# Kernel tuning notes

Measured on AMD Instinct MI355X. Metric: run time of the kernel, lower is better.

## Reference

```python
import jax, jax.numpy as jnp
import numpy as np

D = 64
H = 4
HD = D // H
N_MOL, E_MOL = 2048, 32768
N_PROT, E_PROT = 8192, 262144
LN_EPS = 1e-5


def _lin_params(key, d_in, d_out):
    k1, k2 = jax.random.split(key)
    lim = 1.0 / np.sqrt(d_in)
    w = jax.random.uniform(k1, (d_in, d_out), minval=-lim, maxval=lim, dtype=jnp.float32)
    b = jax.random.uniform(k2, (d_out,), minval=-lim, maxval=lim, dtype=jnp.float32)
    return w, b


def setup_inputs() -> dict:
    key = jax.random.key(0)
    ks = jax.random.split(key, 20)
    inp = {
        'x_mol': jax.random.normal(ks[0], (N_MOL, D), dtype=jnp.float32),
        'edge_index_mol': jax.random.randint(ks[1], (2, E_MOL), 0, N_MOL),
        'edge_attr_mol': jax.random.normal(ks[2], (E_MOL, D), dtype=jnp.float32),
        'x_prot': jax.random.normal(ks[3], (N_PROT, D), dtype=jnp.float32),
        'edge_index_prot': jax.random.randint(ks[4], (2, E_PROT), 0, N_PROT),
        'edge_attr_prot': jax.random.normal(ks[5], (E_PROT, D), dtype=jnp.float32),
    }
    # GINE MLPs: Linear -> ReLU -> Linear
    inp['mol_w1'], inp['mol_b1'] = _lin_params(ks[6], D, D)
    inp['mol_w2'], inp['mol_b2'] = _lin_params(ks[7], D, D)
    inp['prot_w1'], inp['prot_b1'] = _lin_params(ks[8], D, D)
    inp['prot_w2'], inp['prot_b2'] = _lin_params(ks[9], D, D)
    # cross-attn mol->prot (query=mol, key/value=prot)
    inp['mp_wq'], inp['mp_bq'] = _lin_params(ks[10], D, D)
    inp['mp_wk'], inp['mp_bk'] = _lin_params(ks[11], D, D)
    inp['mp_wv'], inp['mp_bv'] = _lin_params(ks[12], D, D)
    # cross-attn prot->mol (query=prot, key/value=mol)
    inp['pm_wq'], inp['pm_bq'] = _lin_params(ks[13], D, D)
    inp['pm_wk'], inp['pm_bk'] = _lin_params(ks[14], D, D)
    inp['pm_wv'], inp['pm_bv'] = _lin_params(ks[15], D, D)
    # layer norms
    inp['ln_mol_g'] = jnp.ones((D,), jnp.float32)
    inp['ln_mol_b'] = jnp.zeros((D,), jnp.float32)
    inp['ln_prot_g'] = jnp.ones((D,), jnp.float32)
    inp['ln_prot_b'] = jnp.zeros((D,), jnp.float32)
    return inp


def _gine_conv(x, edge_index, edge_attr, w1, b1, w2, b2, n_nodes):
    # message: relu(x_j + edge_attr); aggregate: mean at target; update: MLP((1+eps)*x + aggr), eps=0
    src, dst = edge_index[0], edge_index[1]
    msg = jax.nn.relu(x[src] + edge_attr)                       # [E, D]
    ssum = jax.ops.segment_sum(msg, dst, num_segments=n_nodes)  # [N, D]
    cnt = jax.ops.segment_sum(jnp.ones((msg.shape[0],), msg.dtype), dst, num_segments=n_nodes)
    aggr = ssum / jnp.maximum(cnt, 1.0)[:, None]
    h = x + aggr
    h = jax.nn.relu(h @ w1 + b1) @ w2 + b2
    return h


def _cross_attn(q_nodes, k_nodes, wq, bq, wk, bk, wv, bv):
    Nq, Nk = q_nodes.shape[0], k_nodes.shape[0]
    Q = (q_nodes @ wq + bq).reshape(Nq, H, HD)
    K = (k_nodes @ wk + bk).reshape(Nk, H, HD)
    V = (k_nodes @ wv + bv).reshape(Nk, H, HD)
    scores = jnp.einsum('qhd,khd->hqk', Q, K) / np.sqrt(HD).astype(np.float32)
    attn = jax.nn.softmax(scores, axis=-1)                      # [H, Nq, Nk]
    out = jnp.einsum('hqk,khd->qhd', attn, V).reshape(Nq, D)
    return out


def _layer_norm(x, g, b):
    mu = jnp.mean(x, axis=-1, keepdims=True)
    var = jnp.mean(jnp.square(x - mu), axis=-1, keepdims=True)
    return (x - mu) * jax.lax.rsqrt(var + LN_EPS) * g + b


def reference(x_mol, edge_index_mol, edge_attr_mol, x_prot, edge_index_prot, edge_attr_prot,
              mol_w1, mol_b1, mol_w2, mol_b2, prot_w1, prot_b1, prot_w2, prot_b2,
              mp_wq, mp_bq, mp_wk, mp_bk, mp_wv, mp_bv,
              pm_wq, pm_bq, pm_wk, pm_bk, pm_wv, pm_bv,
              ln_mol_g, ln_mol_b, ln_prot_g, ln_prot_b):
    h_mol = jax.nn.relu(_gine_conv(x_mol, edge_index_mol, edge_attr_mol,
                                   mol_w1, mol_b1, mol_w2, mol_b2, x_mol.shape[0]))
    h_prot = jax.nn.relu(_gine_conv(x_prot, edge_index_prot, edge_attr_prot,
                                    prot_w1, prot_b1, prot_w2, prot_b2, x_prot.shape[0]))
    h_mol_attn = _cross_attn(h_mol, h_prot, mp_wq, mp_bq, mp_wk, mp_bk, mp_wv, mp_bv)
    h_prot_attn = _cross_attn(h_prot, h_mol, pm_wq, pm_bq, pm_wk, pm_bk, pm_wv, pm_bv)
    out_mol = _layer_norm(h_mol + h_mol_attn, ln_mol_g, ln_mol_b)
    out_prot = _layer_norm(h_prot + h_prot_attn, ln_prot_g, ln_prot_b)
    return out_mol, out_prot
```

## Files before the change

### kernel.cpp

```cpp
#include <hip/hip_runtime.h>

#define NM 2048
#define EM 32768
#define NP 8192
#define EP 262144

typedef __attribute__((ext_vector_type(8))) short short8;
typedef __attribute__((ext_vector_type(4))) float f32x4;

#define LOG2E 1.44269504088896340736f

__device__ __forceinline__ float e2(float x) { return __builtin_amdgcn_exp2f(x); }
__device__ __forceinline__ unsigned int pk_bf16(float a, float b) {
    unsigned int ua = __float_as_uint(a) + 0x8000u;
    unsigned int ub = __float_as_uint(b) + 0x8000u;
    return __builtin_amdgcn_perm(ua, ub, 0x03020706u);
}
__device__ __forceinline__ unsigned short cvt_bf16(float f) {
    unsigned int u = __float_as_uint(f);
    u = (u + 0x7fff + ((u >> 16) & 1)) >> 16;
    return (unsigned short)u;
}

__global__ __launch_bounds__(256) void hist_kernel(
    const int* __restrict__ ei_m, const int* __restrict__ ei_p,
    int* __restrict__ cnt_m, int* __restrict__ cnt_p)
{
    int idx = blockIdx.x * 256 + threadIdx.x;
    if (idx < EM) atomicAdd(&cnt_m[ei_m[EM + idx]], 1);
    int j = idx - EM;
    if (j >= 0 && j < EP) atomicAdd(&cnt_p[ei_p[EP + j]], 1);
}

__global__ __launch_bounds__(256) void scan_kernel(
    const int* __restrict__ cnt_m, const int* __restrict__ cnt_p,
    int* __restrict__ start_m, int* __restrict__ start_p,
    int* __restrict__ cur_m, int* __restrict__ cur_p)
{
    const int* cnt; int* start; int* cur; int n;
    if (blockIdx.x == 0) { cnt = cnt_m; start = start_m; cur = cur_m; n = NM; }
    else                 { cnt = cnt_p; start = start_p; cur = cur_p; n = NP; }
    int per = n >> 8;
    int tid = threadIdx.x;
    int base = tid * per;
    int s = 0;
    for (int i = 0; i < per; i++) s += cnt[base + i];
    __shared__ int wsum[4];
    int lane = tid & 63, w = tid >> 6;
    int v = s;
    #pragma unroll
    for (int off = 1; off < 64; off <<= 1) {
        int u = __shfl_up(v, off, 64);
        if (lane >= off) v += u;
    }
    if (lane == 63) wsum[w] = v;
    __syncthreads();
    int wo = 0;
    for (int i = 0; i < w; i++) wo += wsum[i];
    int run = wo + v - s;
    for (int i = 0; i < per; i++) {
        start[base + i] = run; cur[base + i] = run;
        run += cnt[base + i];
    }
    if (tid == 255) start[n] = run;
}

__global__ __launch_bounds__(256) void scatter_kernel(
    const int* __restrict__ ei_m, const int* __restrict__ ei_p,
    int* __restrict__ cur_m, int* __restrict__ cur_p,
    int* __restrict__ pidx_m, int* __restrict__ pidx_p)
{
    int idx = blockIdx.x * 256 + threadIdx.x;
    if (idx < EM) {
        int d = ei_m[EM + idx];
        int pos = atomicAdd(&cur_m[d], 1);
        pidx_m[pos] = (idx << 11) | ei_m[idx];
    }
    int j = idx - EM;
    if (j >= 0 && j < EP) {
        int d = ei_p[EP + j];
        int pos = atomicAdd(&cur_p[d], 1);
        pidx_p[pos] = (j << 13) | ei_p[j];
    }
}

__global__ __launch_bounds__(256) void node_aggr_kernel(
    const float* __restrict__ x_m, const float* __restrict__ ea_m,
    const int* __restrict__ start_m, const int* __restrict__ pidx_m,
    const float* __restrict__ x_p, const float* __restrict__ ea_p,
    const int* __restrict__ start_p, const int* __restrict__ pidx_p,
    float* __restrict__ h0_m, float* __restrict__ h0_p)
{
    int wave = threadIdx.x >> 6, lane = threadIdx.x & 63;
    int nid = blockIdx.x * 4 + wave;
    const float *x, *ea; const int *start, *pidx; float* h0; int n, sh, msk;
    if (nid < NM) { x = x_m; ea = ea_m; start = start_m; pidx = pidx_m; h0 = h0_m; n = nid; sh = 11; msk = 2047; }
    else          { x = x_p; ea = ea_p; start = start_p; pidx = pidx_p; h0 = h0_p; n = nid - NM; sh = 13; msk = 8191; }
    int b = start[n], e = start[n + 1];
    int deg = e - b;
    float acc = 0.f;
    for (int c0 = 0; c0 < deg; c0 += 64) {
        int rem = deg - c0;
        int mcount = rem < 64 ? rem : 64;
        int pk = 0;
        if (lane < mcount) pk = pidx[b + c0 + lane];
        int j = 0;
        for (; j + 3 < mcount; j += 4) {
            int v0 = __shfl(pk, j, 64),     v1 = __shfl(pk, j + 1, 64);
            int v2 = __shfl(pk, j + 2, 64), v3 = __shfl(pk, j + 3, 64);
            float a0 = ea[(size_t)(((unsigned)v0) >> sh) * 64 + lane];
            float a1 = ea[(size_t)(((unsigned)v1) >> sh) * 64 + lane];
            float a2 = ea[(size_t)(((unsigned)v2) >> sh) * 64 + lane];
            float a3 = ea[(size_t)(((unsigned)v3) >> sh) * 64 + lane];
            float y0 = x[(size_t)(v0 & msk) * 64 + lane];
            float y1 = x[(size_t)(v1 & msk) * 64 + lane];
            float y2 = x[(size_t)(v2 & msk) * 64 + lane];
            float y3 = x[(size_t)(v3 & msk) * 64 + lane];
            acc += fmaxf(y0 + a0, 0.f);
            acc += fmaxf(y1 + a1, 0.f);
            acc += fmaxf(y2 + a2, 0.f);
            acc += fmaxf(y3 + a3, 0.f);
        }
        for (; j < mcount; ++j) {
            int v0 = __shfl(pk, j, 64);
            acc += fmaxf(x[(size_t)(v0 & msk) * 64 + lane] + ea[(size_t)(((unsigned)v0) >> sh) * 64 + lane], 0.f);
        }
    }
    float aggr = acc / fmaxf((float)deg, 1.f);
    h0[(size_t)n * 64 + lane] = x[(size_t)n * 64 + lane] + aggr;
}

__global__ __launch_bounds__(256) void gine_mlp_kernel(
    const float* __restrict__ h0_m, const float* __restrict__ h0_p,
    const float* __restrict__ w1m, const float* __restrict__ b1m,
    const float* __restrict__ w2m, const float* __restrict__ b2m,
    const float* __restrict__ w1p, const float* __restrict__ b1p,
    const float* __restrict__ w2p, const float* __restrict__ b2p,
    float* __restrict__ hm, float* __restrict__ hp)
{
    const float *h0, *w1, *b1, *w2, *b2; float* out; int row0;
    if (blockIdx.x < NM / 16) {
        h0 = h0_m; w1 = w1m; b1 = b1m; w2 = w2m; b2 = b2m; out = hm;
        row0 = blockIdx.x * 16;
    } else {
        h0 = h0_p; w1 = w1p; b1 = b1p; w2 = w2p; b2 = b2p; out = hp;
        row0 = (blockIdx.x - NM / 16) * 16;
    }
    __shared__ float sW1[4096], sW2[4096], sb1[64], sb2[64];
    __shared__ float sh0[16][64], sh1[16][64];
    int t = threadIdx.x;
    for (int i = t; i < 4096; i += 256) { sW1[i] = w1[i]; sW2[i] = w2[i]; }
    if (t < 64) { sb1[t] = b1[t]; sb2[t] = b2[t]; }
    for (int i = t; i < 16 * 64; i += 256) {
        int r = i >> 6, c = i & 63;
        sh0[r][c] = h0[(size_t)(row0 + r) * 64 + c];
    }
    __syncthreads();
    int j = t & 63, rs = t >> 6;
    for (int r = rs; r < 16; r += 4) {
        float a = sb1[j];
        #pragma unroll
        for (int c = 0; c < 64; c++) a += sh0[r][c] * sW1[c * 64 + j];
        sh1[r][j] = fmaxf(a, 0.0f);
    }
    __syncthreads();
    for (int r = rs; r < 16; r += 4) {
        float a = sb2[j];
        #pragma unroll
        for (int c = 0; c < 64; c++) a += sh1[r][c] * sW2[c * 64 + j];
        out[(size_t)(row0 + r) * 64 + j] = fmaxf(a, 0.0f);
    }
}

__global__ __launch_bounds__(256) void qkv_bf16_kernel(
    const float* __restrict__ hm, const float* __restrict__ hp,
    const float* __restrict__ wq_m, const float* __restrict__ bq_m,
    const float* __restrict__ wk_m, const float* __restrict__ bk_m,
    const float* __restrict__ wv_m, const float* __restrict__ bv_m,
    const float* __restrict__ wq_p, const float* __restrict__ bq_p,
    const float* __restrict__ wk_p, const float* __restrict__ bk_p,
    const float* __restrict__ wv_p, const float* __restrict__ bv_p,
    unsigned short* __restrict__ Qm, unsigned short* __restrict__ Km, unsigned short* __restrict__ Vtm,
    unsigned short* __restrict__ Qp, unsigned short* __restrict__ Kp, unsigned short* __restrict__ Vtp)
{
    const float *x, *wq, *bq, *wk, *bk, *wv, *bv;
    unsigned short *Q, *K, *Vt; int row0, N;
    if (blockIdx.x < NM / 16) {
        x = hm; wq = wq_m; bq = bq_m; wk = wk_m; bk = bk_m; wv = wv_m; bv = bv_m;
        Q = Qm; K = Km; Vt = Vtm; N = NM; row0 = blockIdx.x * 16;
    } else {
        x = hp; wq = wq_p; bq = bq_p; wk = wk_p; bk = bk_p; wv = wv_p; bv = bv_p;
        Q = Qp; K = Kp; Vt = Vtp; N = NP; row0 = (blockIdx.x - NM / 16) * 16;
    }
    __shared__ float sWq[4096], sWk[4096], sWv[4096];
    __shared__ float sbq[64], sbk[64], sbv[64];
    __shared__ float sh0[16][64];
    int t = threadIdx.x;
    for (int i = t; i < 4096; i += 256) { sWq[i] = wq[i]; sWk[i] = wk[i]; sWv[i] = wv[i]; }
    if (t < 64) { sbq[t] = bq[t]; sbk[t] = bk[t]; sbv[t] = bv[t]; }
    for (int i = t; i < 16 * 64; i += 256) {
        int r = i >> 6, c = i & 63;
        sh0[r][c] = x[(size_t)(row0 + r) * 64 + c];
    }
    __syncthreads();
    int j = t & 63, rs = t >> 6;
    for (int r = rs; r < 16; r += 4) {
        float aq = sbq[j], ak = sbk[j], av = sbv[j];
        #pragma unroll
        for (int c = 0; c < 64; c++) {
            float h = sh0[r][c];
            aq += h * sWq[c * 64 + j];
            ak += h * sWk[c * 64 + j];
            av += h * sWv[c * 64 + j];
        }
        size_t o = (size_t)(row0 + r) * 64 + j;
        Q[o] = cvt_bf16(aq * (0.25f * LOG2E));
        K[o] = cvt_bf16(ak);
        Vt[(size_t)j * N + row0 + r] = cvt_bf16(av);
    }
}

__global__ __launch_bounds__(256) void attn_kernel(
    const unsigned short* __restrict__ Qm, const unsigned short* __restrict__ Km,
    const unsigned short* __restrict__ Vtm,
    const unsigned short* __restrict__ Qp, const unsigned short* __restrict__ Kp,
    const unsigned short* __restrict__ Vtp,
    float* __restrict__ partial)
{
    __shared__ unsigned int plds[4][16][20];
    int t = threadIdx.x;
    int wave = t >> 6;
    int lane = t & 63;
    int qrow = lane & 15;
    int quad = lane >> 4;
    int T = blockIdx.x * 4 + wave;

    const unsigned short *Q, *K, *Vt; int Nk, ncb, tloc;
    if (T < 4096) { Q = Qm; K = Kp; Vt = Vtp; Nk = NP; ncb = 3; tloc = T; }
    else          { Q = Qp; K = Km; Vt = Vtm; Nk = NM; ncb = 1; tloc = T - 4096; }
    int chunk = tloc & ((1 << ncb) - 1);
    int tmp = tloc >> ncb;
    int h = tmp & 3;
    int qt = tmp >> 2;

    short8 qf = {};
    if (quad < 2)
        qf = *(const short8*)(Q + ((size_t)(qt * 16 + qrow)) * 64 + h * 16 + quad * 8);

    float m = -3.0e38f, l = 0.0f;
    f32x4 acc = {0.f, 0.f, 0.f, 0.f};
    const f32x4 zero4 = {0.f, 0.f, 0.f, 0.f};
    int kbase = chunk * 1024;
    const unsigned short* vrow = Vt + ((size_t)(h * 16 + qrow)) * Nk;

    short8 kf0n = {}, kf1n = {}, vfn;
    {
        if (quad < 2) {
            kf0n = *(const short8*)(K + ((size_t)(kbase + qrow)) * 64 + h * 16 + quad * 8);
            kf1n = *(const short8*)(K + ((size_t)(kbase + 16 + qrow)) * 64 + h * 16 + quad * 8);
        }
        vfn = *(const short8*)(vrow + kbase + quad * 8);
    }

    for (int it = 0; it < 32; ++it) {
        short8 kf0 = kf0n, kf1 = kf1n, vf = vfn;
        if (it < 31) {
            int key0 = kbase + (it + 1) * 32;
            if (quad < 2) {
                kf0n = *(const short8*)(K + ((size_t)(key0 + qrow)) * 64 + h * 16 + quad * 8);
                kf1n = *(const short8*)(K + ((size_t)(key0 + 16 + qrow)) * 64 + h * 16 + quad * 8);
            }
            vfn = *(const short8*)(vrow + key0 + quad * 8);
        }

        f32x4 s0 = __builtin_amdgcn_mfma_f32_16x16x32_bf16(kf0, qf, zero4, 0, 0, 0);
        f32x4 s1 = __builtin_amdgcn_mfma_f32_16x16x32_bf16(kf1, qf, zero4, 0, 0, 0);

        float tmax = fmaxf(fmaxf(fmaxf(s0.x, s0.y), fmaxf(s0.z, s0.w)),
                           fmaxf(fmaxf(s1.x, s1.y), fmaxf(s1.z, s1.w)));
        tmax = fmaxf(tmax, __shfl_xor(tmax, 16, 64));
        tmax = fmaxf(tmax, __shfl_xor(tmax, 32, 64));
        float mnew = fmaxf(m, tmax);
        float alpha = e2(m - mnew);
        float p00 = e2(s0.x - mnew), p01 = e2(s0.y - mnew);
        float p02 = e2(s0.z - mnew), p03 = e2(s0.w - mnew);
        float p10 = e2(s1.x - mnew), p11 = e2(s1.y - mnew);
        float p12 = e2(s1.z - mnew), p13 = e2(s1.w - mnew);
        l = l * alpha + (((p00 + p01) + (p02 + p03)) + ((p10 + p11) + (p12 + p13)));
        acc.x *= alpha; acc.y *= alpha; acc.z *= alpha; acc.w *= alpha;

        uint2 w0; w0.x = pk_bf16(p00, p01); w0.y = pk_bf16(p02, p03);
        uint2 w1; w1.x = pk_bf16(p10, p11); w1.y = pk_bf16(p12, p13);
        *(uint2*)&plds[wave][qrow][quad * 2] = w0;
        *(uint2*)&plds[wave][qrow][8 + quad * 2] = w1;
        short8 pf = *(short8*)&plds[wave][qrow][quad * 4];

        acc = __builtin_amdgcn_mfma_f32_16x16x32_bf16(vf, pf, acc, 0, 0, 0);
        m = mnew;
    }

    float ltot = l + __shfl_xor(l, 16, 64);
    ltot += __shfl_xor(ltot, 32, 64);

    float* pb = partial + (size_t)T * 288;
    *(f32x4*)&pb[qrow * 16 + quad * 4] = acc;
    if (quad == 0) { pb[256 + qrow] = m; pb[272 + qrow] = ltot; }
}

__global__ __launch_bounds__(256) void merge_ln_kernel(
    const float* __restrict__ partial,
    const float* __restrict__ h_m, const float* __restrict__ h_p,
    const float* __restrict__ gm, const float* __restrict__ bm,
    const float* __restrict__ gp, const float* __restrict__ bp_,
    float* __restrict__ out)
{
    int t = threadIdx.x;
    int grow = blockIdx.x * 4 + (t >> 6);
    int c = t & 63;
    const float *pbase, *hbuf, *g, *bb; float* o; int NC, row;
    if (grow < NM) { pbase = partial;               hbuf = h_m; g = gm; bb = bm;  o = out;             NC = 8; row = grow; }
    else           { pbase = partial + 4096 * 288;  hbuf = h_p; g = gp; bb = bp_; o = out + NM * 64;   NC = 2; row = grow - NM; }
    int hi = c >> 4, d = c & 15;
    int qt = row >> 4, ql = row & 15;
    const float* base = pbase + (size_t)(qt * 4 + hi) * NC * 288;
    float M = -3.0e38f;
    for (int cc = 0; cc < NC; ++cc) M = fmaxf(M, base[cc * 288 + 256 + ql]);
    float L = 0.0f, A = 0.0f;
    for (int cc = 0; cc < NC; ++cc) {
        float w = e2(base[cc * 288 + 256 + ql] - M);
        L += base[cc * 288 + 272 + ql] * w;
        A += base[cc * 288 + ql * 16 + d] * w;
    }
    float v = hbuf[(size_t)row * 64 + c] + A / L;
    float s = v;
    #pragma unroll
    for (int o2 = 32; o2 >= 1; o2 >>= 1) s += __shfl_xor(s, o2, 64);
    float mu = s * (1.0f / 64.0f);
    float dv = v - mu;
    float sq = dv * dv;
    #pragma unroll
    for (int o2 = 32; o2 >= 1; o2 >>= 1) sq += __shfl_xor(sq, o2, 64);
    float var = sq * (1.0f / 64.0f);
    o[(size_t)row * 64 + c] = dv * rsqrtf(var + 1e-5f) * g[c] + bb[c];
}

extern "C" void kernel_launch(void* const* d_in, const int* in_sizes, int n_in,
                              void* d_out, int out_size, void* d_ws, size_t ws_size,
                              hipStream_t stream)
{
    const float* x_mol   = (const float*)d_in[0];
    const int*   ei_mol  = (const int*)  d_in[1];
    const float* ea_mol  = (const float*)d_in[2];
    const float* x_prot  = (const float*)d_in[3];
    const int*   ei_prot = (const int*)  d_in[4];
    const float* ea_prot = (const float*)d_in[5];
    const float* mol_w1  = (const float*)d_in[6];
    const float* mol_b1  = (const float*)d_in[7];
    const float* mol_w2  = (const float*)d_in[8];
    const float* mol_b2  = (const float*)d_in[9];
    const float* prot_w1 = (const float*)d_in[10];
    const float* prot_b1 = (const float*)d_in[11];
    const float* prot_w2 = (const float*)d_in[12];
    const float* prot_b2 = (const float*)d_in[13];
    const float* mp_wq = (const float*)d_in[14]; const float* mp_bq = (const float*)d_in[15];
    const float* mp_wk = (const float*)d_in[16]; const float* mp_bk = (const float*)d_in[17];
    const float* mp_wv = (const float*)d_in[18]; const float* mp_bv = (const float*)d_in[19];
    const float* pm_wq = (const float*)d_in[20]; const float* pm_bq = (const float*)d_in[21];
    const float* pm_wk = (const float*)d_in[22]; const float* pm_bk = (const float*)d_in[23];
    const float* pm_wv = (const float*)d_in[24]; const float* pm_bv = (const float*)d_in[25];
    const float* ln_mol_g  = (const float*)d_in[26];
    const float* ln_mol_b  = (const float*)d_in[27];
    const float* ln_prot_g = (const float*)d_in[28];
    const float* ln_prot_b = (const float*)d_in[29];

    float* ws = (float*)d_ws;
    float* h_mol   = ws;
    float* h_prot  = h_mol + 131072;
    float* partial = h_prot + 524288;
    float* h0_mol  = partial;
    float* h0_prot = h0_mol + 131072;
    int* ip      = (int*)(partial + 2359296);
    int* cnt_m   = ip;
    int* cnt_p   = cnt_m + 2048;
    int* start_m = cnt_p + 8192;
    int* start_p = start_m + 2052;
    int* cur_m   = start_p + 8196;
    int* cur_p   = cur_m + 2048;
    int* pidx_m  = cur_p + 8192;
    int* pidx_p  = pidx_m + 32768;
    unsigned short* bf = (unsigned short*)(pidx_p + 262144);
    unsigned short* Qm  = bf;
    unsigned short* Km  = Qm + 131072;
    unsigned short* Vtm = Km + 131072;
    unsigned short* Qp  = Vtm + 131072;
    unsigned short* Kp  = Qp + 524288;
    unsigned short* Vtp = Kp + 524288;

    hipMemsetAsync(cnt_m, 0, (size_t)(2048 + 8192) * sizeof(int), stream);

    const int EB = (EM + EP) / 256;
    hist_kernel<<<EB, 256, 0, stream>>>(ei_mol, ei_prot, cnt_m, cnt_p);
    scan_kernel<<<2, 256, 0, stream>>>(cnt_m, cnt_p, start_m, start_p, cur_m, cur_p);
    scatter_kernel<<<EB, 256, 0, stream>>>(ei_mol, ei_prot, cur_m, cur_p, pidx_m, pidx_p);
    node_aggr_kernel<<<(NM + NP) / 4, 256, 0, stream>>>(
        x_mol, ea_mol, start_m, pidx_m,
        x_prot, ea_prot, start_p, pidx_p, h0_mol, h0_prot);

    gine_mlp_kernel<<<(NM + NP) / 16, 256, 0, stream>>>(
        h0_mol, h0_prot, mol_w1, mol_b1, mol_w2, mol_b2,
        prot_w1, prot_b1, prot_w2, prot_b2, h_mol, h_prot);

    qkv_bf16_kernel<<<(NM + NP) / 16, 256, 0, stream>>>(
        h_mol, h_prot,
        mp_wq, mp_bq, pm_wk, pm_bk, pm_wv, pm_bv,
        pm_wq, pm_bq, mp_wk, mp_bk, mp_wv, mp_bv,
        Qm, Km, Vtm, Qp, Kp, Vtp);

    attn_kernel<<<2048, 256, 0, stream>>>(Qm, Km, Vtm, Qp, Kp, Vtp, partial);

    float* out = (float*)d_out;
    merge_ln_kernel<<<(NM + NP) / 4, 256, 0, stream>>>(
        partial, h_mol, h_prot, ln_mol_g, ln_mol_b, ln_prot_g, ln_prot_b, out);
}
```

Baseline: 323.3 us.

## Use two-pass exact-max softmax in attention and scalar edge indices in aggregation

The attention kernel now runs a first pass that recomputes QK^T scores to find the exact row max. The second pass then accumulates exp and PV without the online rescale, alpha exp and per-iteration cross-lane shuffles. The node aggregation kernel reads edge indices with wave-uniform scalar loads (readfirstlane) instead of a vector load plus shuffles, and unrolls by 8 for more loads in flight. The cost is a second pass of K loads and score MFMAs in the attention kernel.

```diff
diff --git a/kernel.cpp b/kernel.cpp
--- a/kernel.cpp
+++ b/kernel.cpp
@@ -96,35 +96,45 @@
     const float *x, *ea; const int *start, *pidx; float* h0; int n, sh, msk;
     if (nid < NM) { x = x_m; ea = ea_m; start = start_m; pidx = pidx_m; h0 = h0_m; n = nid; sh = 11; msk = 2047; }
     else          { x = x_p; ea = ea_p; start = start_p; pidx = pidx_p; h0 = h0_p; n = nid - NM; sh = 13; msk = 8191; }
-    int b = start[n], e = start[n + 1];
+    int b  = __builtin_amdgcn_readfirstlane(start[n]);
+    int e  = __builtin_amdgcn_readfirstlane(start[n + 1]);
     int deg = e - b;
+    const int* pp = pidx + b;
     float acc = 0.f;
-    for (int c0 = 0; c0 < deg; c0 += 64) {
-        int rem = deg - c0;
-        int mcount = rem < 64 ? rem : 64;
-        int pk = 0;
-        if (lane < mcount) pk = pidx[b + c0 + lane];
-        int j = 0;
-        for (; j + 3 < mcount; j += 4) {
-            int v0 = __shfl(pk, j, 64),     v1 = __shfl(pk, j + 1, 64);
-            int v2 = __shfl(pk, j + 2, 64), v3 = __shfl(pk, j + 3, 64);
-            float a0 = ea[(size_t)(((unsigned)v0) >> sh) * 64 + lane];
-            float a1 = ea[(size_t)(((unsigned)v1) >> sh) * 64 + lane];
-            float a2 = ea[(size_t)(((unsigned)v2) >> sh) * 64 + lane];
-            float a3 = ea[(size_t)(((unsigned)v3) >> sh) * 64 + lane];
-            float y0 = x[(size_t)(v0 & msk) * 64 + lane];
-            float y1 = x[(size_t)(v1 & msk) * 64 + lane];
-            float y2 = x[(size_t)(v2 & msk) * 64 + lane];
-            float y3 = x[(size_t)(v3 & msk) * 64 + lane];
-            acc += fmaxf(y0 + a0, 0.f);
-            acc += fmaxf(y1 + a1, 0.f);
-            acc += fmaxf(y2 + a2, 0.f);
-            acc += fmaxf(y3 + a3, 0.f);
-        }
-        for (; j < mcount; ++j) {
-            int v0 = __shfl(pk, j, 64);
-            acc += fmaxf(x[(size_t)(v0 & msk) * 64 + lane] + ea[(size_t)(((unsigned)v0) >> sh) * 64 + lane], 0.f);
-        }
+    int j = 0;
+    for (; j + 8 <= deg; j += 8) {
+        int v0 = __builtin_amdgcn_readfirstlane(pp[j]);
+        int v1 = __builtin_amdgcn_readfirstlane(pp[j + 1]);
+        int v2 = __builtin_amdgcn_readfirstlane(pp[j + 2]);
+        int v3 = __builtin_amdgcn_readfirstlane(pp[j + 3]);
+        int v4 = __builtin_amdgcn_readfirstlane(pp[j + 4]);
+        int v5 = __builtin_amdgcn_readfirstlane(pp[j + 5]);
+        int v6 = __builtin_amdgcn_readfirstlane(pp[j + 6]);
+        int v7 = __builtin_amdgcn_readfirstlane(pp[j + 7]);
+        float a0 = ea[(size_t)(((unsigned)v0) >> sh) * 64 + lane];
+        float a1 = ea[(size_t)(((unsigned)v1) >> sh) * 64 + lane];
+        float a2 = ea[(size_t)(((unsigned)v2) >> sh) * 64 + lane];
+        float a3 = ea[(size_t)(((unsigned)v3) >> sh) * 64 + lane];
+        float a4 = ea[(size_t)(((unsigned)v4) >> sh) * 64 + lane];
+        float a5 = ea[(size_t)(((unsigned)v5) >> sh) * 64 + lane];
+        float a6 = ea[(size_t)(((unsigned)v6) >> sh) * 64 + lane];
+        float a7 = ea[(size_t)(((unsigned)v7) >> sh) * 64 + lane];
+        float y0 = x[(size_t)(v0 & msk) * 64 + lane];
+        float y1 = x[(size_t)(v1 & msk) * 64 + lane];
+        float y2 = x[(size_t)(v2 & msk) * 64 + lane];
+        float y3 = x[(size_t)(v3 & msk) * 64 + lane];
+        float y4 = x[(size_t)(v4 & msk) * 64 + lane];
+        float y5 = x[(size_t)(v5 & msk) * 64 + lane];
+        float y6 = x[(size_t)(v6 & msk) * 64 + lane];
+        float y7 = x[(size_t)(v7 & msk) * 64 + lane];
+        acc += fmaxf(y0 + a0, 0.f); acc += fmaxf(y1 + a1, 0.f);
+        acc += fmaxf(y2 + a2, 0.f); acc += fmaxf(y3 + a3, 0.f);
+        acc += fmaxf(y4 + a4, 0.f); acc += fmaxf(y5 + a5, 0.f);
+        acc += fmaxf(y6 + a6, 0.f); acc += fmaxf(y7 + a7, 0.f);
+    }
+    for (; j < deg; ++j) {
+        int v0 = __builtin_amdgcn_readfirstlane(pp[j]);
+        acc += fmaxf(x[(size_t)(v0 & msk) * 64 + lane] + ea[(size_t)(((unsigned)v0) >> sh) * 64 + lane], 0.f);
     }
     float aggr = acc / fmaxf((float)deg, 1.f);
     h0[(size_t)n * 64 + lane] = x[(size_t)n * 64 + lane] + aggr;
@@ -247,47 +257,58 @@
     if (quad < 2)
         qf = *(const short8*)(Q + ((size_t)(qt * 16 + qrow)) * 64 + h * 16 + quad * 8);
 
-    float m = -3.0e38f, l = 0.0f;
-    f32x4 acc = {0.f, 0.f, 0.f, 0.f};
     const f32x4 zero4 = {0.f, 0.f, 0.f, 0.f};
     int kbase = chunk * 1024;
-    const unsigned short* vrow = Vt + ((size_t)(h * 16 + qrow)) * Nk;
+    const unsigned short* krow = K + (size_t)(kbase + qrow) * 64 + h * 16 + quad * 8;
+    const unsigned short* vrow = Vt + ((size_t)(h * 16 + qrow)) * Nk + kbase + quad * 8;
+
+    float mx = -3.0e38f;
+    #pragma unroll 4
+    for (int it = 0; it < 32; ++it) {
+        short8 kf0 = {}, kf1 = {};
+        if (quad < 2) {
+            kf0 = *(const short8*)(krow + (size_t)(it * 32) * 64);
+            kf1 = *(const short8*)(krow + (size_t)(it * 32 + 16) * 64);
+        }
+        f32x4 s0 = __builtin_amdgcn_mfma_f32_16x16x32_bf16(kf0, qf, zero4, 0, 0, 0);
+        f32x4 s1 = __builtin_amdgcn_mfma_f32_16x16x32_bf16(kf1, qf, zero4, 0, 0, 0);
+        float t0 = fmaxf(fmaxf(s0.x, s0.y), fmaxf(s0.z, s0.w));
+        float t1 = fmaxf(fmaxf(s1.x, s1.y), fmaxf(s1.z, s1.w));
+        mx = fmaxf(mx, fmaxf(t0, t1));
+    }
+    mx = fmaxf(mx, __shfl_xor(mx, 16, 64));
+    mx = fmaxf(mx, __shfl_xor(mx, 32, 64));
+    float m = mx;
+
+    float l = 0.0f;
+    f32x4 acc = {0.f, 0.f, 0.f, 0.f};
 
     short8 kf0n = {}, kf1n = {}, vfn;
-    {
-        if (quad < 2) {
-            kf0n = *(const short8*)(K + ((size_t)(kbase + qrow)) * 64 + h * 16 + quad * 8);
-            kf1n = *(const short8*)(K + ((size_t)(kbase + 16 + qrow)) * 64 + h * 16 + quad * 8);
-        }
-        vfn = *(const short8*)(vrow + kbase + quad * 8);
-    }
+    if (quad < 2) {
+        kf0n = *(const short8*)(krow);
+        kf1n = *(const short8*)(krow + 16 * 64);
+    }
+    vfn = *(const short8*)(vrow);
 
     for (int it = 0; it < 32; ++it) {
         short8 kf0 = kf0n, kf1 = kf1n, vf = vfn;
         if (it < 31) {
-            int key0 = kbase + (it + 1) * 32;
+            int off = (it + 1) * 32;
             if (quad < 2) {
-                kf0n = *(const short8*)(K + ((size_t)(key0 + qrow)) * 64 + h * 16 + quad * 8);
-                kf1n = *(const short8*)(K + ((size_t)(key0 + 16 + qrow)) * 64 + h * 16 + quad * 8);
+                kf0n = *(const short8*)(krow + (size_t)off * 64);
+                kf1n = *(const short8*)(krow + (size_t)(off + 16) * 64);
             }
-            vfn = *(const short8*)(vrow + key0 + quad * 8);
+            vfn = *(const short8*)(vrow + off);
         }
 
         f32x4 s0 = __builtin_amdgcn_mfma_f32_16x16x32_bf16(kf0, qf, zero4, 0, 0, 0);
         f32x4 s1 = __builtin_amdgcn_mfma_f32_16x16x32_bf16(kf1, qf, zero4, 0, 0, 0);
 
-        float tmax = fmaxf(fmaxf(fmaxf(s0.x, s0.y), fmaxf(s0.z, s0.w)),
-                           fmaxf(fmaxf(s1.x, s1.y), fmaxf(s1.z, s1.w)));
-        tmax = fmaxf(tmax, __shfl_xor(tmax, 16, 64));
-        tmax = fmaxf(tmax, __shfl_xor(tmax, 32, 64));
-        float mnew = fmaxf(m, tmax);
-        float alpha = e2(m - mnew);
-        float p00 = e2(s0.x - mnew), p01 = e2(s0.y - mnew);
-        float p02 = e2(s0.z - mnew), p03 = e2(s0.w - mnew);
-        float p10 = e2(s1.x - mnew), p11 = e2(s1.y - mnew);
-        float p12 = e2(s1.z - mnew), p13 = e2(s1.w - mnew);
-        l = l * alpha + (((p00 + p01) + (p02 + p03)) + ((p10 + p11) + (p12 + p13)));
-        acc.x *= alpha; acc.y *= alpha; acc.z *= alpha; acc.w *= alpha;
+        float p00 = e2(s0.x - m), p01 = e2(s0.y - m);
+        float p02 = e2(s0.z - m), p03 = e2(s0.w - m);
+        float p10 = e2(s1.x - m), p11 = e2(s1.y - m);
+        float p12 = e2(s1.z - m), p13 = e2(s1.w - m);
+        l += (((p00 + p01) + (p02 + p03)) + ((p10 + p11) + (p12 + p13)));
 
         uint2 w0; w0.x = pk_bf16(p00, p01); w0.y = pk_bf16(p02, p03);
         uint2 w1; w1.x = pk_bf16(p10, p11); w1.y = pk_bf16(p12, p13);
@@ -296,7 +317,6 @@
         short8 pf = *(short8*)&plds[wave][qrow][quad * 4];
 
         acc = __builtin_amdgcn_mfma_f32_16x16x32_bf16(vf, pf, acc, 0, 0, 0);
-        m = mnew;
     }
 
     float ltot = l + __shfl_xor(l, 16, 64);
```

New measurement: 356.6 us. +10.3%, slower.
